# Optimization experiments

Hardware: AMD Instinct MI355X
Metric: run time of the kernel (lower is better)

The kernel has to match this reference:

```python
import jax, jax.numpy as jnp
import numpy as np

N_NODES = 50000
N_EDGES = 800000
D_IN, D_HID, D_OUT = 128, 256, 256


def _sage_conv(x, src, dst, w_l, b_l, w_r, n_nodes):
    # PyG SAGEConv (mean aggr): out = lin_l(mean_{j in N(i)} x_j) + lin_r(x_i)
    # lin_l has bias, lin_r has no bias.
    msg_sum = jax.ops.segment_sum(x[src], dst, num_segments=n_nodes)  # [N, d]
    deg = jax.ops.segment_sum(jnp.ones_like(dst, dtype=x.dtype), dst, num_segments=n_nodes)
    agg = msg_sum / jnp.maximum(deg, 1.0)[:, None]
    return agg @ w_l.T + b_l + x @ w_r.T


def setup_inputs() -> dict:
    key = jax.random.key(0)
    ks = jax.random.split(key, 8)
    x = jax.random.normal(ks[0], (N_NODES, D_IN), dtype=jnp.float32)
    edge_index = jax.random.randint(ks[1], (2, N_EDGES), 0, N_NODES, dtype=jnp.int64)
    s1 = 1.0 / np.sqrt(D_IN)
    s2 = 1.0 / np.sqrt(D_HID)
    w_l1 = jax.random.uniform(ks[2], (D_HID, D_IN), jnp.float32, -s1, s1)
    b_l1 = jax.random.uniform(ks[3], (D_HID,), jnp.float32, -s1, s1)
    w_r1 = jax.random.uniform(ks[4], (D_HID, D_IN), jnp.float32, -s1, s1)
    w_l2 = jax.random.uniform(ks[5], (D_OUT, D_HID), jnp.float32, -s2, s2)
    b_l2 = jax.random.uniform(ks[6], (D_OUT,), jnp.float32, -s2, s2)
    w_r2 = jax.random.uniform(ks[7], (D_OUT, D_HID), jnp.float32, -s2, s2)
    return {"x": x, "edge_index": edge_index,
            "w_l1": w_l1, "b_l1": b_l1, "w_r1": w_r1,
            "w_l2": w_l2, "b_l2": b_l2, "w_r2": w_r2}


def reference(x, edge_index, w_l1, b_l1, w_r1, w_l2, b_l2, w_r2):
    src, dst = edge_index[0], edge_index[1]
    h = jax.nn.relu(_sage_conv(x, src, dst, w_l1, b_l1, w_r1, N_NODES))
    out = jax.nn.relu(_sage_conv(h, src, dst, w_l2, b_l2, w_r2, N_NODES))
    return out
```

## Files before the change

### kernel.cpp

```cpp
#include <hip/hip_runtime.h>
#include <hip/hip_fp16.h>
#include <stdint.h>

#define N_NODES 50000
#define N_EDGES 800000
#define BCAP 64
#define NPART 782
#define NSUB 16
#define SCAP 128

typedef _Float16 f16x8 __attribute__((ext_vector_type(8)));
typedef __attribute__((ext_vector_type(4))) float f32x4;

__device__ __forceinline__ unsigned short f2h(float f) {
    return __builtin_bit_cast(unsigned short, (_Float16)f);
}

__device__ __forceinline__ unsigned char f2fp8o(float v) {
    v = fminf(v, 440.f) + 0.015625f;
    unsigned int u = __builtin_bit_cast(unsigned int, v);
    u += 0x7FFFFu + ((u >> 20) & 1u);
    return (unsigned char)((u >> 20) - 960u);
}

__device__ __forceinline__ void load_lds16(const void* g, void* l) {
    __builtin_amdgcn_global_load_lds(
        (const __attribute__((address_space(1))) void*)(uintptr_t)g,
        (__attribute__((address_space(3))) void*)(unsigned int)(uintptr_t)l,
        16, 0, 0);
}

__global__ __launch_bounds__(256) void part_append_k(
    const int* __restrict__ src, const int* __restrict__ dst,
    int* __restrict__ pcnt, unsigned int* __restrict__ pbuf, int nedges)
{
    int t = blockIdx.x * 256 + threadIdx.x;
    int e0 = t * 4;
    if (e0 >= nedges) return;
    int4 s4 = *(const int4*)(src + e0);
    int4 d4 = *(const int4*)(dst + e0);

    int c0 = (d4.x >> 6) * NSUB + ((e0 + 0) & (NSUB - 1));
    int c1 = (d4.y >> 6) * NSUB + ((e0 + 1) & (NSUB - 1));
    int c2 = (d4.z >> 6) * NSUB + ((e0 + 2) & (NSUB - 1));
    int c3 = (d4.w >> 6) * NSUB + ((e0 + 3) & (NSUB - 1));

    int p0 = atomicAdd(&pcnt[c0 * 16], 1);
    int p1 = atomicAdd(&pcnt[c1 * 16], 1);
    int p2 = atomicAdd(&pcnt[c2 * 16], 1);
    int p3 = atomicAdd(&pcnt[c3 * 16], 1);

    if (p0 < SCAP) pbuf[(size_t)c0 * SCAP + p0] = ((unsigned)(d4.x & 63) << 16) | (unsigned)s4.x;
    if (p1 < SCAP) pbuf[(size_t)c1 * SCAP + p1] = ((unsigned)(d4.y & 63) << 16) | (unsigned)s4.y;
    if (p2 < SCAP) pbuf[(size_t)c2 * SCAP + p2] = ((unsigned)(d4.z & 63) << 16) | (unsigned)s4.z;
    if (p3 < SCAP) pbuf[(size_t)c3 * SCAP + p3] = ((unsigned)(d4.w & 63) << 16) | (unsigned)s4.w;
}

__global__ __launch_bounds__(256) void part_bucket_k(
    const int* __restrict__ pcnt, const unsigned int* __restrict__ pbuf,
    int* __restrict__ bucket, int* __restrict__ degtot, float* __restrict__ invdeg)
{
    __shared__ int lcnt[64];
    int part = blockIdx.x, tid = threadIdx.x;
    int wv = tid >> 6, lane = tid & 63;
    if (tid < 64) lcnt[tid] = 0;
    __syncthreads();
#pragma unroll
    for (int sub = wv; sub < NSUB; sub += 4) {
        int cidx = part * NSUB + sub;
        int n = pcnt[cidx * 16];
        if (n > SCAP) n = SCAP;
        const unsigned int* pb = pbuf + (size_t)cidx * SCAP;
        for (int i = lane; i < n; i += 64) {
            unsigned int en = pb[i];
            int dlow = (int)(en >> 16), s = (int)(en & 0xFFFFu);
            int p = atomicAdd(&lcnt[dlow], 1);
            if (p < BCAP) bucket[(size_t)(part * 64 + dlow) * BCAP + p] = s;
        }
    }
    __syncthreads();
    if (tid < 64) {
        int node = part * 64 + tid;
        if (node < N_NODES) {
            int c = lcnt[tid];
            degtot[node] = (c > BCAP) ? BCAP : c;
            invdeg[node] = 1.0f / (float)(c > 1 ? c : 1);
        }
    }
}

__global__ __launch_bounds__(256) void cvt_x_k(
    const float* __restrict__ x, unsigned short* __restrict__ dst)
{
    int tid = blockIdx.x * 256 + threadIdx.x;
    if (tid >= N_NODES * 32) return;
    int row = tid >> 5, c = (tid & 31) * 4;
    float4 v = *(const float4*)(x + (size_t)row * 128 + c);
    ushort4 o;
    o.x = f2h(v.x); o.y = f2h(v.y); o.z = f2h(v.z); o.w = f2h(v.w);
    *(ushort4*)(dst + (size_t)row * 256 + 128 + c) = o;
}

__global__ __launch_bounds__(256) void cvt_w_k(
    const float* __restrict__ wl, const float* __restrict__ wr,
    unsigned short* __restrict__ dst, int Keach)
{
    int tid = blockIdx.x * 256 + threadIdx.x;
    if (tid >= 256 * 2 * Keach) return;
    int n = tid / (2 * Keach), k = tid - n * 2 * Keach;
    float v = (k < Keach) ? wl[(size_t)n * Keach + k]
                          : wr[(size_t)n * Keach + (k - Keach)];
    dst[tid] = f2h(v);
}

__device__ __forceinline__ void acch4(__half2* a, uint4 u) {
    a[0] = __hadd2(a[0], __builtin_bit_cast(__half2, u.x));
    a[1] = __hadd2(a[1], __builtin_bit_cast(__half2, u.y));
    a[2] = __hadd2(a[2], __builtin_bit_cast(__half2, u.z));
    a[3] = __hadd2(a[3], __builtin_bit_cast(__half2, u.w));
}

__global__ __launch_bounds__(256) void agg1_k(
    const unsigned short* __restrict__ feat,
    const int* __restrict__ bucket, const int* __restrict__ degtot,
    const float* __restrict__ invdeg,
    unsigned short* __restrict__ outmsg)
{
    int wv = threadIdx.x >> 6, lane = threadIdx.x & 63;
    int node = blockIdx.x * 4 + wv;
    if (node >= N_NODES) return;
    int deg = degtot[node];
    int idx0 = bucket[(size_t)node * BCAP + lane];
    const int sub = lane >> 4;
    const int col = lane & 15;

    __half2 acc[4] = {};
    auto rowp = [&](int s) { return (const uint4*)(feat + (size_t)s * 256 + col * 8); };

    int j = 0;
    for (; j + 16 <= deg; j += 16) {
        int s0 = __shfl(idx0, j + sub),     s1 = __shfl(idx0, j + 4 + sub);
        int s2 = __shfl(idx0, j + 8 + sub), s3 = __shfl(idx0, j + 12 + sub);
        uint4 u0 = *rowp(s0), u1 = *rowp(s1), u2 = *rowp(s2), u3 = *rowp(s3);
        acch4(acc, u0); acch4(acc, u1); acch4(acc, u2); acch4(acc, u3);
    }
    for (; j + 8 <= deg; j += 8) {
        int s0 = __shfl(idx0, j + sub), s1 = __shfl(idx0, j + 4 + sub);
        uint4 u0 = *rowp(s0), u1 = *rowp(s1);
        acch4(acc, u0); acch4(acc, u1);
    }
    for (; j + 4 <= deg; j += 4) {
        uint4 u0 = *rowp(__shfl(idx0, j + sub));
        acch4(acc, u0);
    }
    if (j < deg) {
        int e = j + sub;
        int ec = (e < deg) ? e : (deg - 1);
        uint4 u0 = *rowp(__shfl(idx0, ec));
        if (e < deg) acch4(acc, u0);
    }
#pragma unroll
    for (int stride = 32; stride >= 16; stride >>= 1)
#pragma unroll
        for (int v = 0; v < 4; v++) {
            int t = __shfl_xor(__builtin_bit_cast(int, acc[v]), stride);
            acc[v] = __hadd2(acc[v], __builtin_bit_cast(__half2, t));
        }

    if (lane < 16) {
        float s = invdeg[node];
        unsigned int o[4];
#pragma unroll
        for (int v = 0; v < 4; v++) {
            float2 f = __half22float2(acc[v]);
            o[v] = (unsigned int)f2h(f.x * s) | ((unsigned int)f2h(f.y * s) << 16);
        }
        *(uint4*)(outmsg + (size_t)node * 256 + lane * 8) = make_uint4(o[0], o[1], o[2], o[3]);
    }
}

__device__ __forceinline__ void accf8pk(__half2* a, unsigned int w) {
    unsigned int ev = ((w & 0x00FF00FFu) << 7) + 0x20002000u;
    unsigned int od = ((w >> 1) & 0x7F807F80u) + 0x20002000u;
    a[0] = __hadd2(a[0], __builtin_bit_cast(__half2, ev));
    a[1] = __hadd2(a[1], __builtin_bit_cast(__half2, od));
}
__device__ __forceinline__ void accf8x16(__half2* a, uint4 u) {
    accf8pk(a + 0, u.x); accf8pk(a + 2, u.y); accf8pk(a + 4, u.z); accf8pk(a + 6, u.w);
}

__global__ __launch_bounds__(256) void agg2_k(
    const unsigned char* __restrict__ hf8,
    const int* __restrict__ bucket, const int* __restrict__ degtot,
    const float* __restrict__ invdeg,
    unsigned short* __restrict__ outmsg)
{
    int wv = threadIdx.x >> 6, lane = threadIdx.x & 63;
    int node = blockIdx.x * 4 + wv;
    if (node >= N_NODES) return;
    int deg = degtot[node];
    int idx0 = bucket[(size_t)node * BCAP + lane];
    const int sub = lane >> 4;
    const int col = lane & 15;

    __half2 acc[8] = {};
    auto rowp = [&](int s) { return (const uint4*)(hf8 + (size_t)s * 256 + col * 16); };

    int j = 0;
    for (; j + 16 <= deg; j += 16) {
        int s0 = __shfl(idx0, j + sub),     s1 = __shfl(idx0, j + 4 + sub);
        int s2 = __shfl(idx0, j + 8 + sub), s3 = __shfl(idx0, j + 12 + sub);
        uint4 u0 = *rowp(s0), u1 = *rowp(s1), u2 = *rowp(s2), u3 = *rowp(s3);
        accf8x16(acc, u0); accf8x16(acc, u1); accf8x16(acc, u2); accf8x16(acc, u3);
    }
    for (; j + 8 <= deg; j += 8) {
        int s0 = __shfl(idx0, j + sub), s1 = __shfl(idx0, j + 4 + sub);
        uint4 u0 = *rowp(s0), u1 = *rowp(s1);
        accf8x16(acc, u0); accf8x16(acc, u1);
    }
    for (; j + 4 <= deg; j += 4) {
        uint4 u0 = *rowp(__shfl(idx0, j + sub));
        accf8x16(acc, u0);
    }
    if (j < deg) {
        int e = j + sub;
        int ec = (e < deg) ? e : (deg - 1);
        uint4 u0 = *rowp(__shfl(idx0, ec));
        if (e < deg) accf8x16(acc, u0);
    }
#pragma unroll
    for (int stride = 32; stride >= 16; stride >>= 1)
#pragma unroll
        for (int v = 0; v < 8; v++) {
            int t = __shfl_xor(__builtin_bit_cast(int, acc[v]), stride);
            acc[v] = __hadd2(acc[v], __builtin_bit_cast(__half2, t));
        }

    if (lane < 16) {
        float s = invdeg[node];
        float bias = (deg > 0) ? 0.015625f : 0.0f;
        unsigned int o[8];
#pragma unroll
        for (int q = 0; q < 4; q++) {
            float2 ev = __half22float2(acc[2 * q]);
            float2 od = __half22float2(acc[2 * q + 1]);
            float d0 = ev.x * s - bias, d1 = od.x * s - bias;
            float d2 = ev.y * s - bias, d3 = od.y * s - bias;
            o[2 * q]     = (unsigned int)f2h(d0) | ((unsigned int)f2h(d1) << 16);
            o[2 * q + 1] = (unsigned int)f2h(d2) | ((unsigned int)f2h(d3) << 16);
        }
        unsigned short* wp = outmsg + (size_t)node * 512 + lane * 16;
        *(uint4*)(wp)     = make_uint4(o[0], o[1], o[2], o[3]);
        *(uint4*)(wp + 8) = make_uint4(o[4], o[5], o[6], o[7]);
    }
}

template <bool F16OUT, bool WRITE_FP8, int K>
__global__ __launch_bounds__(256) void gemm_k(
    const unsigned short* __restrict__ A, const unsigned short* __restrict__ W,
    const float* __restrict__ bias, void* __restrict__ outp, int outStride,
    unsigned char* __restrict__ hf8, int M)
{
    constexpr int NITER = K / 32;
    __shared__ __align__(16) char smem[NITER * 4096];

    const int t = threadIdx.x;
    const int wv = t >> 6, lane = t & 63;
    const int quad = lane >> 4, l15 = lane & 15;
    const int col0 = blockIdx.x * 64;
    const int row0 = blockIdx.y * 256 + wv * 64;

#pragma unroll
    for (int n = 0; n < NITER; n++) {
        int c = n * 256 + t;
        int cl = c & 63, tt = (c >> 6) & 3, ki = c >> 8;
        load_lds16(W + (size_t)(col0 + tt * 16 + (cl & 15)) * K + ki * 32 + (cl >> 4) * 8,
                   smem + c * 16);
    }

    const unsigned short* pA[4];
#pragma unroll
    for (int rg = 0; rg < 4; rg++) {
        int r = row0 + rg * 16 + l15;
        if (r > M - 1) r = M - 1;
        pA[rg] = A + (size_t)r * K + quad * 8;
    }

    f16x8 ab[4][4];
#pragma unroll
    for (int rg = 0; rg < 4; rg++) ab[0][rg] = *(const f16x8*)(pA[rg]);
#pragma unroll
    for (int rg = 0; rg < 4; rg++) ab[1][rg] = *(const f16x8*)(pA[rg] + 32);

    __syncthreads();

    f32x4 acc[4][4] = {};
#pragma unroll
    for (int i = 0; i < NITER; i++) {
        if (i + 2 < NITER) {
#pragma unroll
            for (int rg = 0; rg < 4; rg++)
                ab[(i + 2) & 3][rg] = *(const f16x8*)(pA[rg] + (i + 2) * 32);
        }
        const char* wb = smem + i * 4096 + lane * 16;
#pragma unroll
        for (int tt = 0; tt < 4; tt++) {
            f16x8 b = *(const f16x8*)(wb + tt * 1024);
#pragma unroll
            for (int rg = 0; rg < 4; rg++)
                acc[rg][tt] = __builtin_amdgcn_mfma_f32_16x16x32_f16(
                    ab[i & 3][rg], b, acc[rg][tt], 0, 0, 0);
        }
    }

#pragma unroll
    for (int tt = 0; tt < 4; tt++) {
        int col = col0 + tt * 16 + l15;
        float bv = bias[col];
#pragma unroll
        for (int rg = 0; rg < 4; rg++) {
#pragma unroll
            for (int ii = 0; ii < 4; ii++) {
                int row = row0 + rg * 16 + quad * 4 + ii;
                if (row < M) {
                    float v = fmaxf(acc[rg][tt][ii] + bv, 0.f);
                    size_t off = (size_t)row * outStride + col;
                    if constexpr (F16OUT) ((unsigned short*)outp)[off] = f2h(v);
                    else                  ((float*)outp)[off] = v;
                    if constexpr (WRITE_FP8) hf8[(size_t)row * 256 + col] = f2fp8o(v);
                }
            }
        }
    }
}

extern "C" void kernel_launch(void* const* d_in, const int* in_sizes, int n_in,
                              void* d_out, int out_size, void* d_ws, size_t ws_size,
                              hipStream_t stream)
{
    const float* x   = (const float*)d_in[0];
    const int*   ei  = (const int*)d_in[1];
    const float* wl1 = (const float*)d_in[2];
    const float* bl1 = (const float*)d_in[3];
    const float* wr1 = (const float*)d_in[4];
    const float* wl2 = (const float*)d_in[5];
    const float* bl2 = (const float*)d_in[6];
    const float* wr2 = (const float*)d_in[7];
    float* out = (float*)d_out;
    const int* src = ei;
    const int* dst = ei + N_EDGES;

    char* ws = (char*)d_ws;
    size_t off = 0;
    auto alloc = [&](size_t bytes) -> void* {
        void* p = ws + off;
        off = (off + bytes + 255) & ~(size_t)255;
        return p;
    };
    int*            pcnt   = (int*)           alloc((size_t)NPART * NSUB * 16 * 4);
    unsigned int*   pbuf   = (unsigned int*)  alloc((size_t)NPART * NSUB * SCAP * 4);
    int*            bucket = (int*)           alloc((size_t)NPART * 64 * BCAP * 4);
    int*            degtot = (int*)           alloc((size_t)N_NODES * 4);
    float*          invdeg = (float*)         alloc((size_t)N_NODES * 4);
    unsigned short* Acat1  = (unsigned short*)alloc((size_t)N_NODES * 256 * 2);
    unsigned short* Acat2  = (unsigned short*)alloc((size_t)N_NODES * 512 * 2);
    unsigned char*  hf8    = (unsigned char*) alloc((size_t)N_NODES * 256);
    unsigned short* Wcat1  = (unsigned short*)alloc((size_t)256 * 256 * 2);
    unsigned short* Wcat2  = (unsigned short*)alloc((size_t)256 * 512 * 2);

    hipMemsetAsync(pcnt, 0, (size_t)NPART * NSUB * 16 * 4, stream);
    part_append_k<<<(N_EDGES / 4 + 255) / 256, 256, 0, stream>>>(src, dst, pcnt, pbuf, N_EDGES);
    part_bucket_k<<<NPART, 256, 0, stream>>>(pcnt, pbuf, bucket, degtot, invdeg);

    cvt_x_k<<<(N_NODES * 32 + 255) / 256, 256, 0, stream>>>(x, Acat1);
    cvt_w_k<<<(256 * 256 + 255) / 256, 256, 0, stream>>>(wl1, wr1, Wcat1, 128);
    cvt_w_k<<<(256 * 512 + 255) / 256, 256, 0, stream>>>(wl2, wr2, Wcat2, 256);

    agg1_k<<<(N_NODES + 3) / 4, 256, 0, stream>>>(
        Acat1 + 128, bucket, degtot, invdeg, Acat1);
    gemm_k<true, true, 256><<<dim3(4, (N_NODES + 255) / 256), 256, 0, stream>>>(
        Acat1, Wcat1, bl1, (void*)(Acat2 + 256), 512, hf8, N_NODES);

    agg2_k<<<(N_NODES + 3) / 4, 256, 0, stream>>>(
        hf8, bucket, degtot, invdeg, Acat2);
    gemm_k<false, false, 512><<<dim3(4, (N_NODES + 255) / 256), 256, 0, stream>>>(
        Acat2, Wcat2, bl2, (void*)out, 256, nullptr, N_NODES);
}
```

Baseline: 314.3 us.

## Pre-swizzle weights into MFMA fragment order and stream them from global into registers

The weight-conversion kernel now writes W in the exact per-lane fragment order the MFMA loop consumes, so the GEMM loads B operands straight from global/L2 into registers with double buffering. This removes the LDS staging, the global_load_lds copy and the block-wide barrier. The GEMM grid is also remapped to a 1D swizzled order so that 8 row tiles and 4 column tiles run close together for better L2 reuse of A. In exchange every wave reloads its weights from cache instead of sharing them through LDS, which adds global traffic and register pressure.

```diff
diff --git a/kernel.cpp b/kernel.cpp
--- a/kernel.cpp
+++ b/kernel.cpp
@@ -21,13 +21,6 @@
     unsigned int u = __builtin_bit_cast(unsigned int, v);
     u += 0x7FFFFu + ((u >> 20) & 1u);
     return (unsigned char)((u >> 20) - 960u);
-}
-
-__device__ __forceinline__ void load_lds16(const void* g, void* l) {
-    __builtin_amdgcn_global_load_lds(
-        (const __attribute__((address_space(1))) void*)(uintptr_t)g,
-        (__attribute__((address_space(3))) void*)(unsigned int)(uintptr_t)l,
-        16, 0, 0);
 }
 
 __global__ __launch_bounds__(256) void part_append_k(
@@ -101,15 +94,19 @@
     *(ushort4*)(dst + (size_t)row * 256 + 128 + c) = o;
 }
 
-__global__ __launch_bounds__(256) void cvt_w_k(
+__global__ __launch_bounds__(256) void cvt_wf_k(
     const float* __restrict__ wl, const float* __restrict__ wr,
     unsigned short* __restrict__ dst, int Keach)
 {
+    int K = 2 * Keach, NITER = K >> 5;
     int tid = blockIdx.x * 256 + threadIdx.x;
-    if (tid >= 256 * 2 * Keach) return;
-    int n = tid / (2 * Keach), k = tid - n * 2 * Keach;
-    float v = (k < Keach) ? wl[(size_t)n * Keach + k]
-                          : wr[(size_t)n * Keach + (k - Keach)];
+    if (tid >= 256 * K) return;
+    int j = tid & 7, lane = (tid >> 3) & 63, tt = (tid >> 9) & 3, rest = tid >> 11;
+    int i = rest % NITER, p = rest / NITER;
+    int col = p * 64 + tt * 16 + (lane & 15);
+    int k = i * 32 + (lane >> 4) * 8 + j;
+    float v = (k < Keach) ? wl[(size_t)col * Keach + k]
+                          : wr[(size_t)col * Keach + (k - Keach)];
     dst[tid] = f2h(v);
 }
 
@@ -257,42 +254,39 @@
 
 template <bool F16OUT, bool WRITE_FP8, int K>
 __global__ __launch_bounds__(256) void gemm_k(
-    const unsigned short* __restrict__ A, const unsigned short* __restrict__ W,
+    const unsigned short* __restrict__ A, const unsigned short* __restrict__ Wf,
     const float* __restrict__ bias, void* __restrict__ outp, int outStride,
     unsigned char* __restrict__ hf8, int M)
 {
     constexpr int NITER = K / 32;
-    __shared__ __align__(16) char smem[NITER * 4096];
+    const int id = blockIdx.x;
+    const int r  = (id >> 5) * 8 + (id & 7);
+    const int p  = (id >> 3) & 3;
+    const int NR = (M + 255) >> 8;
+    if (r >= NR) return;
 
     const int t = threadIdx.x;
     const int wv = t >> 6, lane = t & 63;
     const int quad = lane >> 4, l15 = lane & 15;
-    const int col0 = blockIdx.x * 64;
-    const int row0 = blockIdx.y * 256 + wv * 64;
-
-#pragma unroll
-    for (int n = 0; n < NITER; n++) {
-        int c = n * 256 + t;
-        int cl = c & 63, tt = (c >> 6) & 3, ki = c >> 8;
-        load_lds16(W + (size_t)(col0 + tt * 16 + (cl & 15)) * K + ki * 32 + (cl >> 4) * 8,
-                   smem + c * 16);
-    }
+    const int col0 = p * 64;
+    const int row0 = r * 256 + wv * 64;
 
     const unsigned short* pA[4];
 #pragma unroll
     for (int rg = 0; rg < 4; rg++) {
-        int r = row0 + rg * 16 + l15;
-        if (r > M - 1) r = M - 1;
-        pA[rg] = A + (size_t)r * K + quad * 8;
-    }
-
-    f16x8 ab[4][4];
+        int rr = row0 + rg * 16 + l15;
+        if (rr > M - 1) rr = M - 1;
+        pA[rg] = A + (size_t)rr * K + quad * 8;
+    }
+    const unsigned short* pW = Wf + (size_t)p * NITER * 2048 + lane * 8;
+
+    f16x8 ab[3][4], wb[2][4];
 #pragma unroll
     for (int rg = 0; rg < 4; rg++) ab[0][rg] = *(const f16x8*)(pA[rg]);
 #pragma unroll
     for (int rg = 0; rg < 4; rg++) ab[1][rg] = *(const f16x8*)(pA[rg] + 32);
-
-    __syncthreads();
+#pragma unroll
+    for (int tt = 0; tt < 4; tt++) wb[0][tt] = *(const f16x8*)(pW + tt * 512);
 
     f32x4 acc[4][4] = {};
 #pragma unroll
@@ -300,17 +294,19 @@
         if (i + 2 < NITER) {
 #pragma unroll
             for (int rg = 0; rg < 4; rg++)
-                ab[(i + 2) & 3][rg] = *(const f16x8*)(pA[rg] + (i + 2) * 32);
-        }
-        const char* wb = smem + i * 4096 + lane * 16;
-#pragma unroll
-        for (int tt = 0; tt < 4; tt++) {
-            f16x8 b = *(const f16x8*)(wb + tt * 1024);
+                ab[(i + 2) % 3][rg] = *(const f16x8*)(pA[rg] + (i + 2) * 32);
+        }
+        if (i + 1 < NITER) {
+#pragma unroll
+            for (int tt = 0; tt < 4; tt++)
+                wb[(i + 1) & 1][tt] = *(const f16x8*)(pW + (i + 1) * 2048 + tt * 512);
+        }
+#pragma unroll
+        for (int tt = 0; tt < 4; tt++)
 #pragma unroll
             for (int rg = 0; rg < 4; rg++)
                 acc[rg][tt] = __builtin_amdgcn_mfma_f32_16x16x32_f16(
-                    ab[i & 3][rg], b, acc[rg][tt], 0, 0, 0);
-        }
+                    ab[i % 3][rg], wb[i & 1][tt], acc[rg][tt], 0, 0, 0);
     }
 
 #pragma unroll
@@ -365,24 +361,27 @@
     unsigned short* Acat1  = (unsigned short*)alloc((size_t)N_NODES * 256 * 2);
     unsigned short* Acat2  = (unsigned short*)alloc((size_t)N_NODES * 512 * 2);
     unsigned char*  hf8    = (unsigned char*) alloc((size_t)N_NODES * 256);
-    unsigned short* Wcat1  = (unsigned short*)alloc((size_t)256 * 256 * 2);
-    unsigned short* Wcat2  = (unsigned short*)alloc((size_t)256 * 512 * 2);
+    unsigned short* Wf1    = (unsigned short*)alloc((size_t)256 * 256 * 2);
+    unsigned short* Wf2    = (unsigned short*)alloc((size_t)256 * 512 * 2);
+
+    const int NRB = (N_NODES + 255) / 256;
+    const int GEMM_BLOCKS = 32 * ((NRB + 7) / 8);
 
     hipMemsetAsync(pcnt, 0, (size_t)NPART * NSUB * 16 * 4, stream);
     part_append_k<<<(N_EDGES / 4 + 255) / 256, 256, 0, stream>>>(src, dst, pcnt, pbuf, N_EDGES);
     part_bucket_k<<<NPART, 256, 0, stream>>>(pcnt, pbuf, bucket, degtot, invdeg);
 
     cvt_x_k<<<(N_NODES * 32 + 255) / 256, 256, 0, stream>>>(x, Acat1);
-    cvt_w_k<<<(256 * 256 + 255) / 256, 256, 0, stream>>>(wl1, wr1, Wcat1, 128);
-    cvt_w_k<<<(256 * 512 + 255) / 256, 256, 0, stream>>>(wl2, wr2, Wcat2, 256);
+    cvt_wf_k<<<256, 256, 0, stream>>>(wl1, wr1, Wf1, 128);
+    cvt_wf_k<<<512, 256, 0, stream>>>(wl2, wr2, Wf2, 256);
 
     agg1_k<<<(N_NODES + 3) / 4, 256, 0, stream>>>(
         Acat1 + 128, bucket, degtot, invdeg, Acat1);
-    gemm_k<true, true, 256><<<dim3(4, (N_NODES + 255) / 256), 256, 0, stream>>>(
-        Acat1, Wcat1, bl1, (void*)(Acat2 + 256), 512, hf8, N_NODES);
+    gemm_k<true, true, 256><<<GEMM_BLOCKS, 256, 0, stream>>>(
+        Acat1, Wf1, bl1, (void*)(Acat2 + 256), 512, hf8, N_NODES);
 
     agg2_k<<<(N_NODES + 3) / 4, 256, 0, stream>>>(
         hf8, bucket, degtot, invdeg, Acat2);
-    gemm_k<false, false, 512><<<dim3(4, (N_NODES + 255) / 256), 256, 0, stream>>>(
-        Acat2, Wcat2, bl2, (void*)out, 256, nullptr, N_NODES);
-}
+    gemm_k<false, false, 512><<<GEMM_BLOCKS, 256, 0, stream>>>(
+        Acat2, Wf2, bl2, (void*)out, 256, nullptr, N_NODES);
+}
```

After: 317.6 us. Within noise of the previous version (+1.1%).
